# Kernel optimization log

Hardware: AMD Instinct MI355X
Metric: run time of the kernel (lower is better)

The kernel has to match this reference:

```python
import jax, jax.numpy as jnp
import numpy as np

T, M, HW = 16, 256, 1024
D_MODEL, D_K, H = 512, 512, 8
HEAD = D_K // H
SIGMA = 0.5
EPS = 1e-6

def layernorm_nobias(x, gamma):
    mu = jnp.mean(x, axis=-1, keepdims=True)
    var = jnp.mean((x - mu) ** 2, axis=-1, keepdims=True)
    return (x - mu) * jax.lax.rsqrt(var + EPS) * gamma

def setup_inputs() -> dict:
    key = jax.random.key(0)
    ks = jax.random.split(key, 11)
    s = 0.02
    return {
        "updated_track_tokens": jax.random.normal(ks[0], (T, M, D_MODEL), jnp.float32),
        "tracks": jax.random.uniform(ks[1], (T, M, 2), jnp.float32) * 32.0,
        "feature_positions": jax.random.uniform(ks[2], (HW, 2), jnp.float32) * 32.0,
        "feature_pos_embeddings": jax.random.normal(ks[3], (T, HW, D_MODEL), jnp.float32),
        "track_pos_embeddings": jax.random.normal(ks[4], (T, M, D_MODEL), jnp.float32),
        "W_q": jax.random.normal(ks[5], (D_K, D_MODEL), jnp.float32) * s,
        "W_k": jax.random.normal(ks[6], (D_K, D_MODEL), jnp.float32) * s,
        "W_v": jax.random.normal(ks[7], (D_MODEL, D_MODEL), jnp.float32) * s,
        "W_out": jax.random.normal(ks[8], (D_MODEL, D_MODEL), jnp.float32) * s,
        "q_gamma": jnp.ones((D_K,), jnp.float32),
        "k_gamma": jnp.ones((D_K,), jnp.float32),
    }

def reference(updated_track_tokens, tracks, feature_positions, feature_pos_embeddings,
              track_pos_embeddings, W_q, W_k, W_v, W_out, q_gamma, k_gamma):
    # Projections (torch Linear: x @ W.T)
    Q = feature_pos_embeddings @ W_q.T       # [T, HW, D_K]
    K = track_pos_embeddings @ W_k.T         # [T, M, D_K]
    V = updated_track_tokens @ W_v.T         # [T, M, D_MODEL]
    # QK LayerNorm (no bias) over full d_k, before head split
    Q = layernorm_nobias(Q, q_gamma)
    K = layernorm_nobias(K, k_gamma)
    Qh = Q.reshape(T, HW, H, HEAD).transpose(0, 2, 1, 3)          # [T,H,HW,hd]
    Kh = K.reshape(T, M, H, HEAD).transpose(0, 2, 1, 3)           # [T,H,M,hd]
    Vh = V.reshape(T, M, H, D_MODEL // H).transpose(0, 2, 1, 3)   # [T,H,M,dv]
    scores = jnp.einsum('thqd,thkd->thqk', Qh, Kh) / np.float32(np.sqrt(HEAD))
    # Vectorized spatial bias: squared euclidean distance feat->track per t
    diff = feature_positions[None, :, None, :] - tracks[:, None, :, :]  # [T,HW,M,2]
    d2 = jnp.sum(diff * diff, axis=-1)                                  # [T,HW,M]
    bias = -d2 / (2.0 * SIGMA ** 2)
    scores = scores + bias[:, None, :, :]                               # broadcast heads
    attn = jax.nn.softmax(scores, axis=-1)
    upd = jnp.einsum('thqk,thkd->thqd', attn, Vh)                       # [T,H,HW,dv]
    upd = upd.transpose(0, 2, 1, 3).reshape(T, HW, D_MODEL)
    return upd @ W_out.T
```

## Files before the change

### kernel.cpp

```cpp
#include <hip/hip_runtime.h>

#define T_    16
#define M_    256
#define HW_   1024
#define DM    512
#define H_    8
#define HEAD_ 64
#define LOG2E 1.4426950408889634f

typedef __attribute__((ext_vector_type(8))) short short8;
typedef __attribute__((ext_vector_type(4))) float f32x4;

__device__ __forceinline__ unsigned cvtpk(float lo, float hi) {
    unsigned r;
    asm("v_cvt_pk_bf16_f32 %0, %1, %2" : "=v"(r) : "v"(lo), "v"(hi));
    return r;
}

__device__ __forceinline__ float fexp2(float x) {
    float r;
    asm("v_exp_f32 %0, %1\n\ts_nop 1" : "=v"(r) : "v"(x));
    return r;
}

__device__ __forceinline__ float b2f(unsigned short u) {
    return __uint_as_float(((unsigned)u) << 16);
}

__device__ __forceinline__ void gload16(const void* g, void* l) {
    __builtin_amdgcn_global_load_lds(
        (const __attribute__((address_space(1))) void*)g,
        (__attribute__((address_space(3))) void*)l, 16, 0, 0);
}

__global__ __launch_bounds__(256) void cvtall(const float* __restrict__ fpe,
                                              const float* __restrict__ tpe,
                                              const float* __restrict__ utt,
                                              const float* __restrict__ Wq,
                                              const float* __restrict__ Wk,
                                              const float* __restrict__ Wv,
                                              const float* __restrict__ Wo,
                                              unsigned short* __restrict__ Fb,
                                              unsigned short* __restrict__ Tb,
                                              unsigned short* __restrict__ Ub0,
                                              unsigned short* __restrict__ Wbf) {
    size_t e = (size_t)(blockIdx.x * 256 + threadIdx.x) * 8;
    const float* s;
    unsigned short* d;
    if (e < 8388608)        { s = fpe + e;              d = Fb  + e; }
    else if (e < 10485760)  { s = tpe + (e - 8388608);  d = Tb  + (e - 8388608); }
    else if (e < 12582912)  { s = utt + (e - 10485760); d = Ub0 + (e - 10485760); }
    else if (e < 12845056)  { s = Wq  + (e - 12582912); d = Wbf + (e - 12582912 + 0); }
    else if (e < 13107200)  { s = Wk  + (e - 12845056); d = Wbf + (e - 12845056 + 262144); }
    else if (e < 13369344)  { s = Wv  + (e - 13107200); d = Wbf + (e - 13107200 + 524288); }
    else                    { s = Wo  + (e - 13369344); d = Wbf + (e - 13369344 + 786432); }
    float4 a = *reinterpret_cast<const float4*>(s);
    float4 b = *reinterpret_cast<const float4*>(s + 4);
    uint4 v = make_uint4(cvtpk(a.x, a.y), cvtpk(a.z, a.w),
                         cvtpk(b.x, b.y), cvtpk(b.z, b.w));
    *reinterpret_cast<uint4*>(d) = v;
}

__global__ __launch_bounds__(256) void proj3(const unsigned short* __restrict__ Fb,
                                             const unsigned short* __restrict__ Tb,
                                             const unsigned short* __restrict__ Ub0,
                                             const unsigned short* __restrict__ Wbf,
                                             unsigned short* __restrict__ Qb,
                                             unsigned short* __restrict__ Kb,
                                             unsigned short* __restrict__ Vb) {
    __shared__ __align__(16) unsigned char smem[24576];
    unsigned char* As = smem;
    unsigned char* Bs = smem + 8192;

    const int b  = blockIdx.x;
    const int x  = b & 7;
    const int cp = (b >> 3) & 3;
    const int m  = b >> 5;
    const int p  = x * 48 + m;
    const unsigned short *X, *W;
    unsigned short* C;
    int r0;
    if (p < 256)      { X = Fb;  W = Wbf;          C = Qb; r0 = p * 64; }
    else if (p < 320) { X = Tb;  W = Wbf + 262144; C = Kb; r0 = (p - 256) * 64; }
    else              { X = Ub0; W = Wbf + 524288; C = Vb; r0 = (p - 320) * 64; }
    const int c0 = cp * 128;

    const int tid = threadIdx.x;
    const int l  = tid & 63;
    const int wid = tid >> 6;
    const int wr = wid >> 1, wc = wid & 1;
    const int g = l >> 4;
    const int c = l & 15;

    f32x4 acc[2][4] = {};

    for (int k0 = 0; k0 < DM; k0 += 64) {
        #pragma unroll
        for (int i = 0; i < 2; ++i) {
            int idx = tid + i * 256;
            int row = idx >> 3, jj = idx & 7;
            int j = jj ^ (row & 7);
            gload16(X + (size_t)(r0 + row) * DM + k0 + j * 8, As + idx * 16);
        }
        #pragma unroll
        for (int i = 0; i < 4; ++i) {
            int idx = tid + i * 256;
            int row = idx >> 3, jj = idx & 7;
            int j = jj ^ (row & 7);
            gload16(W + (size_t)(c0 + row) * DM + k0 + j * 8, Bs + idx * 16);
        }
        __syncthreads();

        #pragma unroll
        for (int ks = 0; ks < 2; ++ks) {
            short8 af[2], bfr[4];
            #pragma unroll
            for (int mm = 0; mm < 2; ++mm) {
                int rq = wr * 32 + mm * 16 + c;
                af[mm] = *reinterpret_cast<short8*>(
                    As + ((rq * 128 + ks * 64 + g * 16) ^ ((rq & 7) << 4)));
            }
            #pragma unroll
            for (int n = 0; n < 4; ++n) {
                int rn = wc * 64 + n * 16 + c;
                bfr[n] = *reinterpret_cast<short8*>(
                    Bs + ((rn * 128 + ks * 64 + g * 16) ^ ((rn & 7) << 4)));
            }
            #pragma unroll
            for (int mm = 0; mm < 2; ++mm)
                #pragma unroll
                for (int n = 0; n < 4; ++n)
                    acc[mm][n] = __builtin_amdgcn_mfma_f32_16x16x32_bf16(
                        af[mm], bfr[n], acc[mm][n], 0, 0, 0);
        }
        __syncthreads();
    }

    #pragma unroll
    for (int mm = 0; mm < 2; ++mm)
        #pragma unroll
        for (int n = 0; n < 4; ++n)
            #pragma unroll
            for (int r = 0; r < 4; ++r)
                C[(size_t)(r0 + wr * 32 + mm * 16 + g * 4 + r) * DM +
                  c0 + wc * 64 + n * 16 + c] =
                    (unsigned short)cvtpk(acc[mm][n][r], acc[mm][n][r]);
}

__global__ __launch_bounds__(256) void gemm_bb(const unsigned short* __restrict__ X,
                                               const unsigned short* __restrict__ W,
                                               float* __restrict__ C) {
    __shared__ __align__(16) unsigned char smem[24576];
    unsigned char* As = smem;
    unsigned char* Bs = smem + 8192;

    const int b  = blockIdx.x;
    const int x  = b & 7;
    const int cp = (b >> 3) & 3;
    const int m  = b >> 5;
    const int p  = x * 32 + m;
    const int r0 = p * 64;
    const int c0 = cp * 128;

    const int tid = threadIdx.x;
    const int l  = tid & 63;
    const int wid = tid >> 6;
    const int wr = wid >> 1, wc = wid & 1;
    const int g = l >> 4;
    const int c = l & 15;

    f32x4 acc[2][4] = {};

    for (int k0 = 0; k0 < DM; k0 += 64) {
        #pragma unroll
        for (int i = 0; i < 2; ++i) {
            int idx = tid + i * 256;
            int row = idx >> 3, jj = idx & 7;
            int j = jj ^ (row & 7);
            gload16(X + (size_t)(r0 + row) * DM + k0 + j * 8, As + idx * 16);
        }
        #pragma unroll
        for (int i = 0; i < 4; ++i) {
            int idx = tid + i * 256;
            int row = idx >> 3, jj = idx & 7;
            int j = jj ^ (row & 7);
            gload16(W + (size_t)(c0 + row) * DM + k0 + j * 8, Bs + idx * 16);
        }
        __syncthreads();

        #pragma unroll
        for (int ks = 0; ks < 2; ++ks) {
            short8 af[2], bfr[4];
            #pragma unroll
            for (int mm = 0; mm < 2; ++mm) {
                int rq = wr * 32 + mm * 16 + c;
                af[mm] = *reinterpret_cast<short8*>(
                    As + ((rq * 128 + ks * 64 + g * 16) ^ ((rq & 7) << 4)));
            }
            #pragma unroll
            for (int n = 0; n < 4; ++n) {
                int rn = wc * 64 + n * 16 + c;
                bfr[n] = *reinterpret_cast<short8*>(
                    Bs + ((rn * 128 + ks * 64 + g * 16) ^ ((rn & 7) << 4)));
            }
            #pragma unroll
            for (int mm = 0; mm < 2; ++mm)
                #pragma unroll
                for (int n = 0; n < 4; ++n)
                    acc[mm][n] = __builtin_amdgcn_mfma_f32_16x16x32_bf16(
                        af[mm], bfr[n], acc[mm][n], 0, 0, 0);
        }
        __syncthreads();
    }

    #pragma unroll
    for (int mm = 0; mm < 2; ++mm)
        #pragma unroll
        for (int n = 0; n < 4; ++n)
            #pragma unroll
            for (int r = 0; r < 4; ++r)
                C[(size_t)(r0 + wr * 32 + mm * 16 + g * 4 + r) * DM +
                  c0 + wc * 64 + n * 16 + c] = acc[mm][n][r];
}

__global__ __launch_bounds__(256) void normpack(const unsigned short* __restrict__ Qb,
                                                const unsigned short* __restrict__ Kb,
                                                const unsigned short* __restrict__ Vb,
                                                const float* __restrict__ qg,
                                                const float* __restrict__ kg,
                                                unsigned short* __restrict__ Qbf,
                                                unsigned short* __restrict__ Kbf,
                                                unsigned short* __restrict__ Vt) {
    __shared__ unsigned short vtile[64][68];
    const int bid = blockIdx.x;
    const int tid = threadIdx.x;

    if (bid < 5120) {
        const unsigned short* X; const float* gamma; unsigned short* Y;
        int rowbase; float sc;
        if (bid < 4096) { X = Qb; gamma = qg; Y = Qbf; rowbase = bid * 4; sc = 0.125f * LOG2E; }
        else            { X = Kb; gamma = kg; Y = Kbf; rowbase = (bid - 4096) * 4; sc = 1.0f; }

        const int wave = tid / 64;
        const int lane = tid % 64;
        const int row  = rowbase + wave;

        short8 xv = *reinterpret_cast<const short8*>(&X[(size_t)row * DM + lane * 8]);
        float x[8];
        #pragma unroll
        for (int i = 0; i < 8; ++i) x[i] = b2f((unsigned short)xv[i]);

        float s = 0.f;
        #pragma unroll
        for (int i = 0; i < 8; ++i) s += x[i];
        #pragma unroll
        for (int m = 1; m < 64; m <<= 1) s += __shfl_xor(s, m, 64);
        const float mu = s * (1.0f / 512.0f);

        float vs = 0.f;
        #pragma unroll
        for (int i = 0; i < 8; ++i) { float d = x[i] - mu; vs += d * d; }
        #pragma unroll
        for (int m = 1; m < 64; m <<= 1) vs += __shfl_xor(vs, m, 64);
        const float rs = rsqrtf(vs * (1.0f / 512.0f) + 1e-6f) * sc;

        float4 g0 = *reinterpret_cast<const float4*>(&gamma[lane * 8]);
        float4 g1 = *reinterpret_cast<const float4*>(&gamma[lane * 8 + 4]);
        float gv[8] = {g0.x, g0.y, g0.z, g0.w, g1.x, g1.y, g1.z, g1.w};

        float y[8];
        #pragma unroll
        for (int i = 0; i < 8; ++i) y[i] = (x[i] - mu) * rs * gv[i];
        uint4 o = make_uint4(cvtpk(y[0], y[1]), cvtpk(y[2], y[3]),
                             cvtpk(y[4], y[5]), cvtpk(y[6], y[7]));
        *reinterpret_cast<uint4*>(&Y[(size_t)row * DM + lane * 8]) = o;
    } else {
        const int b2 = bid - 5120;
        const int dt = b2 & 7, kt = (b2 >> 3) & 3, t = b2 >> 5;

        #pragma unroll
        for (int i = 0; i < 4; ++i) {
            int idx = tid + i * 256;
            int r = idx >> 4, c4 = idx & 15;
            uint2 v = *reinterpret_cast<const uint2*>(
                &Vb[(size_t)(t * M_ + kt * 64 + r) * DM + dt * 64 + c4 * 4]);
            *reinterpret_cast<uint2*>(&vtile[r][c4 * 4]) = v;
        }
        __syncthreads();
        #pragma unroll
        for (int i = 0; i < 4; ++i) {
            int idx = tid + i * 256;
            int r = idx >> 4, c4 = idx & 15;
            unsigned a0 = vtile[c4 * 4 + 0][r], a1 = vtile[c4 * 4 + 1][r];
            unsigned a2 = vtile[c4 * 4 + 2][r], a3 = vtile[c4 * 4 + 3][r];
            uint2 o = make_uint2(a0 | (a1 << 16), a2 | (a3 << 16));
            *reinterpret_cast<uint2*>(
                &Vt[((size_t)t * DM + dt * 64 + r) * M_ + kt * 64 + c4 * 4]) = o;
        }
    }
}

__global__ __launch_bounds__(512, 4) void attn_mfma(const unsigned short* __restrict__ Qbf,
                                                    const unsigned short* __restrict__ Kbf,
                                                    const unsigned short* __restrict__ VtG,
                                                    const float* __restrict__ tracks,
                                                    const float* __restrict__ fpos,
                                                    unsigned short* __restrict__ Ubf) {
    const int b   = blockIdx.x;
    const int xcd = b & 7;
    const int bi  = b >> 3;
    const int qt  = bi & 7;
    const int pp  = xcd + (bi >> 3) * 8;
    const int t   = pp >> 3;
    const int h   = pp & 7;
    const int q0  = qt * 128;
    const int tid = threadIdx.x;

    __shared__ __align__(16) unsigned char smem[32768 + 3072 + 1024];
    unsigned char* KV = smem;
    float* tx4 = (float*)(smem + 32768);
    float* ty4 = (float*)(smem + 32768 + 1024);
    float* tz2 = (float*)(smem + 32768 + 2048);
    float* fps = (float*)(smem + 32768 + 3072);

    const int l  = tid & 63;
    const int wq = tid >> 6;
    const int g  = l >> 4;
    const int c  = l & 15;

    const unsigned short* qrow =
        Qbf + (size_t)(t * HW_ + q0 + wq * 16 + c) * DM + h * HEAD_;
    short8 bQ0 = *reinterpret_cast<const short8*>(qrow + g * 8);
    short8 bQ1 = *reinterpret_cast<const short8*>(qrow + 32 + g * 8);

    #pragma unroll
    for (int it = 0; it < 4; ++it) {
        int idx = tid + it * 512;
        int row = idx >> 3, jj = idx & 7;
        int j = jj ^ (row & 7);
        gload16(Kbf + (size_t)(t * M_ + row) * DM + h * HEAD_ + j * 8, KV + idx * 16);
    }
    if (tid < 256) {
        float2 tk = *reinterpret_cast<const float2*>(&tracks[t * 512 + tid * 2]);
        tx4[tid] = tk.x * (4.0f * LOG2E);
        ty4[tid] = tk.y * (4.0f * LOG2E);
        tz2[tid] = -2.0f * LOG2E * (tk.x * tk.x + tk.y * tk.y);
        fps[tid] = fpos[q0 * 2 + tid];
    }
    __syncthreads();

    f32x4 acc[16];
    __builtin_amdgcn_s_setprio(1);
    #pragma unroll
    for (int n = 0; n < 16; ++n) {
        int rk = n * 16 + c;
        short8 a0 = *reinterpret_cast<short8*>(KV + ((rk * 128 + g * 16) ^ ((rk & 7) << 4)));
        short8 a1 = *reinterpret_cast<short8*>(KV + ((rk * 128 + 64 + g * 16) ^ ((rk & 7) << 4)));
        f32x4 z = {0.f, 0.f, 0.f, 0.f};
        z = __builtin_amdgcn_mfma_f32_16x16x32_bf16(a0, bQ0, z, 0, 0, 0);
        z = __builtin_amdgcn_mfma_f32_16x16x32_bf16(a1, bQ1, z, 0, 0, 0);
        acc[n] = z;
    }
    __builtin_amdgcn_s_setprio(0);

    __syncthreads();

    #pragma unroll
    for (int it = 0; it < 4; ++it) {
        int idx = tid + it * 512;
        int row = idx >> 5, kcc = idx & 31;
        int kc = kcc ^ (row & 7);
        gload16(VtG + ((size_t)t * DM + h * HEAD_ + row) * M_ + kc * 8, KV + idx * 16);
    }

    const float fx = fps[(wq * 16 + c) * 2];
    const float fy = fps[(wq * 16 + c) * 2 + 1];
    const float fz = -2.0f * LOG2E * (fx * fx + fy * fy);
    unsigned pk[16][2];
    float vr[16];
    #pragma unroll
    for (int n = 0; n < 16; ++n) {
        float4 x4 = *reinterpret_cast<float4*>(&tx4[n * 16 + g * 4]);
        float4 y4 = *reinterpret_cast<float4*>(&ty4[n * 16 + g * 4]);
        float4 z4 = *reinterpret_cast<float4*>(&tz2[n * 16 + g * 4]);
        float e0 = fexp2((acc[n][0] + fz) + fmaf(fx, x4.x, fmaf(fy, y4.x, z4.x)));
        float e1 = fexp2((acc[n][1] + fz) + fmaf(fx, x4.y, fmaf(fy, y4.y, z4.y)));
        float e2 = fexp2((acc[n][2] + fz) + fmaf(fx, x4.z, fmaf(fy, y4.z, z4.z)));
        float e3 = fexp2((acc[n][3] + fz) + fmaf(fx, x4.w, fmaf(fy, y4.w, z4.w)));
        pk[n][0] = cvtpk(e0, e1);
        pk[n][1] = cvtpk(e2, e3);
        vr[n] = (e0 + e1) + (e2 + e3);
    }

    #pragma unroll
    for (int s = 8; s >= 1; s >>= 1)
        #pragma unroll
        for (int n = 0; n < 8; ++n)
            if (n < s) vr[n] += vr[n + s];
    float sum = vr[0];
    sum += __shfl_xor(sum, 16, 64);
    sum += __shfl_xor(sum, 32, 64);
    const float inv = 1.0f / sum;

    float invr[4];
    #pragma unroll
    for (int r = 0; r < 4; ++r)
        invr[r] = __shfl(inv, (l & 48) | ((l >> 2) & 12) | r, 64);

    __syncthreads();

    f32x4 o[4] = {{0.f,0.f,0.f,0.f},{0.f,0.f,0.f,0.f},{0.f,0.f,0.f,0.f},{0.f,0.f,0.f,0.f}};
    __builtin_amdgcn_s_setprio(1);
    #pragma unroll
    for (int ks = 0; ks < 8; ++ks) {
        unsigned wb[4];
        #pragma unroll
        for (int wt = 0; wt < 4; ++wt) {
            int src = ((l & 16) << 1) + (wt >> 1) * 16 + c;
            unsigned ve = (unsigned)__shfl((int)pk[2 * ks][wt & 1], src, 64);
            unsigned vo = (unsigned)__shfl((int)pk[2 * ks + 1][wt & 1], src, 64);
            wb[wt] = (g < 2) ? ve : vo;
        }
        uint4 uu = make_uint4(wb[0], wb[1], wb[2], wb[3]);
        short8 aP = *reinterpret_cast<short8*>(&uu);
        #pragma unroll
        for (int nv = 0; nv < 4; ++nv) {
            int rv = nv * 16 + c;
            short8 bV = *reinterpret_cast<short8*>(
                KV + ((rv * 512 + ks * 64 + g * 16) ^ ((rv & 7) << 4)));
            o[nv] = __builtin_amdgcn_mfma_f32_16x16x32_bf16(aP, bV, o[nv], 0, 0, 0);
        }
    }
    __builtin_amdgcn_s_setprio(0);

    #pragma unroll
    for (int nv = 0; nv < 4; ++nv)
        #pragma unroll
        for (int r = 0; r < 4; ++r) {
            float xo = o[nv][r] * invr[r];
            Ubf[(size_t)(t * HW_ + q0 + wq * 16 + g * 4 + r) * DM +
                h * HEAD_ + nv * 16 + c] = (unsigned short)cvtpk(xo, xo);
        }
}

extern "C" void kernel_launch(void* const* d_in, const int* in_sizes, int n_in,
                              void* d_out, int out_size, void* d_ws, size_t ws_size,
                              hipStream_t stream) {
    const float* utt    = (const float*)d_in[0];
    const float* tracks = (const float*)d_in[1];
    const float* fpos   = (const float*)d_in[2];
    const float* fpe    = (const float*)d_in[3];
    const float* tpe    = (const float*)d_in[4];
    const float* Wq     = (const float*)d_in[5];
    const float* Wk     = (const float*)d_in[6];
    const float* Wv     = (const float*)d_in[7];
    const float* Wo     = (const float*)d_in[8];
    const float* qgamma = (const float*)d_in[9];
    const float* kgamma = (const float*)d_in[10];
    float* out = (float*)d_out;

    char* ws = (char*)d_ws;
    unsigned short* Fb  = (unsigned short*)(ws);
    unsigned short* Tb  = (unsigned short*)(ws + 16777216);
    unsigned short* Ub0 = (unsigned short*)(ws + 20971520);
    unsigned short* Qb  = (unsigned short*)(ws + 25165824);
    unsigned short* Kb  = (unsigned short*)(ws + 41943040);
    unsigned short* Vb  = (unsigned short*)(ws + 46137344);
    unsigned short* Qbf = (unsigned short*)(ws + 50331648);
    unsigned short* Kbf = (unsigned short*)(ws + 67108864);
    unsigned short* Vt  = (unsigned short*)(ws + 71303168);
    unsigned short* Wbf = (unsigned short*)(ws + 75497472);
    unsigned short* Ubf = (unsigned short*)(ws);

    cvtall<<<6656, 256, 0, stream>>>(fpe, tpe, utt, Wq, Wk, Wv, Wo, Fb, Tb, Ub0, Wbf);

    proj3<<<1536, 256, 0, stream>>>(Fb, Tb, Ub0, Wbf, Qb, Kb, Vb);

    normpack<<<5632, 256, 0, stream>>>(Qb, Kb, Vb, qgamma, kgamma, Qbf, Kbf, Vt);

    attn_mfma<<<1024, 512, 0, stream>>>(Qbf, Kbf, Vt, tracks, fpos, Ubf);

    gemm_bb<<<1024, 256, 0, stream>>>(Ubf, Wbf + 786432, out);
}
```

Before: 89.33 us.

## Fold Q layernorm into attention scores using per-row stats and K-gamma sums

Stops writing a normalized bf16 copy of Q. normpack now stores only per-row mean and rstd for Q. K is normalized with both gammas folded in, and per-head sums of the normalized K are stored. The attention kernel reads raw Q and rebuilds the normalized score algebraically as aq*dot + bq*ksum, which removes a 16MB write and its reread. In exchange it adds an extra FMA and LDS read per score, and precision changes because the raw, unnormalized Q goes through bf16 MFMA.

```diff
diff --git a/kernel.cpp b/kernel.cpp
--- a/kernel.cpp
+++ b/kernel.cpp
@@ -228,24 +228,20 @@
                                                 const unsigned short* __restrict__ Vb,
                                                 const float* __restrict__ qg,
                                                 const float* __restrict__ kg,
-                                                unsigned short* __restrict__ Qbf,
+                                                float* __restrict__ Qst,
                                                 unsigned short* __restrict__ Kbf,
+                                                float* __restrict__ kgs,
                                                 unsigned short* __restrict__ Vt) {
     __shared__ unsigned short vtile[64][68];
     const int bid = blockIdx.x;
     const int tid = threadIdx.x;
 
-    if (bid < 5120) {
-        const unsigned short* X; const float* gamma; unsigned short* Y;
-        int rowbase; float sc;
-        if (bid < 4096) { X = Qb; gamma = qg; Y = Qbf; rowbase = bid * 4; sc = 0.125f * LOG2E; }
-        else            { X = Kb; gamma = kg; Y = Kbf; rowbase = (bid - 4096) * 4; sc = 1.0f; }
-
+    if (bid < 4096) {
         const int wave = tid / 64;
         const int lane = tid % 64;
-        const int row  = rowbase + wave;
-
-        short8 xv = *reinterpret_cast<const short8*>(&X[(size_t)row * DM + lane * 8]);
+        const int row  = bid * 4 + wave;
+
+        short8 xv = *reinterpret_cast<const short8*>(&Qb[(size_t)row * DM + lane * 8]);
         float x[8];
         #pragma unroll
         for (int i = 0; i < 8; ++i) x[i] = b2f((unsigned short)xv[i]);
@@ -262,18 +258,57 @@
         for (int i = 0; i < 8; ++i) { float d = x[i] - mu; vs += d * d; }
         #pragma unroll
         for (int m = 1; m < 64; m <<= 1) vs += __shfl_xor(vs, m, 64);
-        const float rs = rsqrtf(vs * (1.0f / 512.0f) + 1e-6f) * sc;
-
-        float4 g0 = *reinterpret_cast<const float4*>(&gamma[lane * 8]);
-        float4 g1 = *reinterpret_cast<const float4*>(&gamma[lane * 8 + 4]);
+        const float rs = rsqrtf(vs * (1.0f / 512.0f) + 1e-6f);
+
+        if (lane == 0)
+            *reinterpret_cast<float2*>(&Qst[(size_t)row * 2]) = make_float2(mu, rs);
+    } else if (bid < 5120) {
+        const int wave = tid / 64;
+        const int lane = tid % 64;
+        const int row  = (bid - 4096) * 4 + wave;
+
+        short8 xv = *reinterpret_cast<const short8*>(&Kb[(size_t)row * DM + lane * 8]);
+        float x[8];
+        #pragma unroll
+        for (int i = 0; i < 8; ++i) x[i] = b2f((unsigned short)xv[i]);
+
+        float s = 0.f;
+        #pragma unroll
+        for (int i = 0; i < 8; ++i) s += x[i];
+        #pragma unroll
+        for (int m = 1; m < 64; m <<= 1) s += __shfl_xor(s, m, 64);
+        const float mu = s * (1.0f / 512.0f);
+
+        float vs = 0.f;
+        #pragma unroll
+        for (int i = 0; i < 8; ++i) { float d = x[i] - mu; vs += d * d; }
+        #pragma unroll
+        for (int m = 1; m < 64; m <<= 1) vs += __shfl_xor(vs, m, 64);
+        const float rs = rsqrtf(vs * (1.0f / 512.0f) + 1e-6f);
+
+        float4 g0 = *reinterpret_cast<const float4*>(&kg[lane * 8]);
+        float4 g1 = *reinterpret_cast<const float4*>(&kg[lane * 8 + 4]);
         float gv[8] = {g0.x, g0.y, g0.z, g0.w, g1.x, g1.y, g1.z, g1.w};
+        float4 q0v = *reinterpret_cast<const float4*>(&qg[lane * 8]);
+        float4 q1v = *reinterpret_cast<const float4*>(&qg[lane * 8 + 4]);
+        float qv[8] = {q0v.x, q0v.y, q0v.z, q0v.w, q1v.x, q1v.y, q1v.z, q1v.w};
 
         float y[8];
-        #pragma unroll
-        for (int i = 0; i < 8; ++i) y[i] = (x[i] - mu) * rs * gv[i];
+        float part = 0.f;
+        #pragma unroll
+        for (int i = 0; i < 8; ++i) {
+            y[i] = (x[i] - mu) * rs * gv[i] * qv[i];
+            part += y[i];
+        }
         uint4 o = make_uint4(cvtpk(y[0], y[1]), cvtpk(y[2], y[3]),
                              cvtpk(y[4], y[5]), cvtpk(y[6], y[7]));
-        *reinterpret_cast<uint4*>(&Y[(size_t)row * DM + lane * 8]) = o;
+        *reinterpret_cast<uint4*>(&Kbf[(size_t)row * DM + lane * 8]) = o;
+
+        part += __shfl_xor(part, 1, 64);
+        part += __shfl_xor(part, 2, 64);
+        part += __shfl_xor(part, 4, 64);
+        if ((lane & 7) == 0)
+            kgs[(size_t)row * 8 + (lane >> 3)] = part;
     } else {
         const int b2 = bid - 5120;
         const int dt = b2 & 7, kt = (b2 >> 3) & 3, t = b2 >> 5;
@@ -300,8 +335,10 @@
     }
 }
 
-__global__ __launch_bounds__(512, 4) void attn_mfma(const unsigned short* __restrict__ Qbf,
+__global__ __launch_bounds__(512, 4) void attn_mfma(const unsigned short* __restrict__ Qb,
+                                                    const float* __restrict__ Qst,
                                                     const unsigned short* __restrict__ Kbf,
+                                                    const float* __restrict__ kgs,
                                                     const unsigned short* __restrict__ VtG,
                                                     const float* __restrict__ tracks,
                                                     const float* __restrict__ fpos,
@@ -316,12 +353,13 @@
     const int q0  = qt * 128;
     const int tid = threadIdx.x;
 
-    __shared__ __align__(16) unsigned char smem[32768 + 3072 + 1024];
+    __shared__ __align__(16) unsigned char smem[32768 + 4096 + 1024];
     unsigned char* KV = smem;
     float* tx4 = (float*)(smem + 32768);
     float* ty4 = (float*)(smem + 32768 + 1024);
     float* tz2 = (float*)(smem + 32768 + 2048);
-    float* fps = (float*)(smem + 32768 + 3072);
+    float* kg4 = (float*)(smem + 32768 + 3072);
+    float* fps = (float*)(smem + 32768 + 4096);
 
     const int l  = tid & 63;
     const int wq = tid >> 6;
@@ -329,9 +367,13 @@
     const int c  = l & 15;
 
     const unsigned short* qrow =
-        Qbf + (size_t)(t * HW_ + q0 + wq * 16 + c) * DM + h * HEAD_;
+        Qb + (size_t)(t * HW_ + q0 + wq * 16 + c) * DM + h * HEAD_;
     short8 bQ0 = *reinterpret_cast<const short8*>(qrow + g * 8);
     short8 bQ1 = *reinterpret_cast<const short8*>(qrow + 32 + g * 8);
+    float2 st = *reinterpret_cast<const float2*>(
+        &Qst[(size_t)(t * HW_ + q0 + wq * 16 + c) * 2]);
+    const float aq = 0.125f * LOG2E * st.y;
+    const float bq = -st.x * aq;
 
     #pragma unroll
     for (int it = 0; it < 4; ++it) {
@@ -345,6 +387,7 @@
         tx4[tid] = tk.x * (4.0f * LOG2E);
         ty4[tid] = tk.y * (4.0f * LOG2E);
         tz2[tid] = -2.0f * LOG2E * (tk.x * tk.x + tk.y * tk.y);
+        kg4[tid] = kgs[(size_t)(t * M_ + tid) * 8 + h];
         fps[tid] = fpos[q0 * 2 + tid];
     }
     __syncthreads();
@@ -383,10 +426,15 @@
         float4 x4 = *reinterpret_cast<float4*>(&tx4[n * 16 + g * 4]);
         float4 y4 = *reinterpret_cast<float4*>(&ty4[n * 16 + g * 4]);
         float4 z4 = *reinterpret_cast<float4*>(&tz2[n * 16 + g * 4]);
-        float e0 = fexp2((acc[n][0] + fz) + fmaf(fx, x4.x, fmaf(fy, y4.x, z4.x)));
-        float e1 = fexp2((acc[n][1] + fz) + fmaf(fx, x4.y, fmaf(fy, y4.y, z4.y)));
-        float e2 = fexp2((acc[n][2] + fz) + fmaf(fx, x4.z, fmaf(fy, y4.z, z4.z)));
-        float e3 = fexp2((acc[n][3] + fz) + fmaf(fx, x4.w, fmaf(fy, y4.w, z4.w)));
+        float4 k4 = *reinterpret_cast<float4*>(&kg4[n * 16 + g * 4]);
+        float e0 = fexp2(fmaf(aq, acc[n][0],
+                    fz + fmaf(bq, k4.x, fmaf(fx, x4.x, fmaf(fy, y4.x, z4.x)))));
+        float e1 = fexp2(fmaf(aq, acc[n][1],
+                    fz + fmaf(bq, k4.y, fmaf(fx, x4.y, fmaf(fy, y4.y, z4.y)))));
+        float e2 = fexp2(fmaf(aq, acc[n][2],
+                    fz + fmaf(bq, k4.z, fmaf(fx, x4.z, fmaf(fy, y4.z, z4.z)))));
+        float e3 = fexp2(fmaf(aq, acc[n][3],
+                    fz + fmaf(bq, k4.w, fmaf(fx, x4.w, fmaf(fy, y4.w, z4.w)))));
         pk[n][0] = cvtpk(e0, e1);
         pk[n][1] = cvtpk(e2, e3);
         vr[n] = (e0 + e1) + (e2 + e3);
@@ -466,7 +514,8 @@
     unsigned short* Qb  = (unsigned short*)(ws + 25165824);
     unsigned short* Kb  = (unsigned short*)(ws + 41943040);
     unsigned short* Vb  = (unsigned short*)(ws + 46137344);
-    unsigned short* Qbf = (unsigned short*)(ws + 50331648);
+    float*          Qst = (float*)(ws + 50331648);
+    float*          kgs = (float*)(ws + 50462720);
     unsigned short* Kbf = (unsigned short*)(ws + 67108864);
     unsigned short* Vt  = (unsigned short*)(ws + 71303168);
     unsigned short* Wbf = (unsigned short*)(ws + 75497472);
@@ -476,9 +525,9 @@
 
     proj3<<<1536, 256, 0, stream>>>(Fb, Tb, Ub0, Wbf, Qb, Kb, Vb);
 
-    normpack<<<5632, 256, 0, stream>>>(Qb, Kb, Vb, qgamma, kgamma, Qbf, Kbf, Vt);
-
-    attn_mfma<<<1024, 512, 0, stream>>>(Qbf, Kbf, Vt, tracks, fpos, Ubf);
+    normpack<<<5632, 256, 0, stream>>>(Qb, Kb, Vb, qgamma, kgamma, Qst, Kbf, kgs, Vt);
+
+    attn_mfma<<<1024, 512, 0, stream>>>(Qb, Qst, Kbf, kgs, Vt, tracks, fpos, Ubf);
 
     gemm_bb<<<1024, 256, 0, stream>>>(Ubf, Wbf + 786432, out);
 }
```

After: 92.10 us. +3.1%, slower.
